# Optimization experiments

Hardware: AMD Instinct MI355X
Metric: run time of the kernel (lower is better)

The kernel has to match this reference:

```python
import math
import jax, jax.numpy as jnp
import numpy as np

B, S, H = 2, 2048, 1024
NH = 16
HD = H // NH            # 64
ROT = int(HD * 0.25)    # 16
QKV_SLOTS = 1024
PROJ_SLOTS = 1024
FFN_SLOTS = 4096
EPS = 1e-5


def gelu_l2_norm(x, axis=-1):
    # F.gelu (exact erf) then L2-normalize and rescale by sqrt(dim)
    g = jax.nn.gelu(x, approximate=False)
    n = jnp.linalg.norm(g, ord=2, axis=axis, keepdims=True)
    return g / n * math.sqrt(g.shape[axis])


def layer_norm(x, w, b):
    mu = jnp.mean(x, axis=-1, keepdims=True)
    var = jnp.mean(jnp.square(x - mu), axis=-1, keepdims=True)
    return (x - mu) * jax.lax.rsqrt(var + EPS) * w + b


def pattention(x, key_tok, val_tok):
    # [.., in] @ [slots, in]^T -> [.., slots]; NOTE: scale MULTIPLIES (as in source)
    aw = jnp.einsum('bsh,ph->bsp', x, key_tok) * math.sqrt(x.shape[-1])
    aw = gelu_l2_norm(aw, axis=-1)
    return jnp.einsum('bsp,pd->bsd', aw, val_tok)


def rotary_cos_sin(seq_len, rot_dim, base=10000.0):
    inv_freq = 1.0 / (base ** (jnp.arange(0, rot_dim, 2, dtype=jnp.float32) / rot_dim))
    t = jnp.arange(seq_len, dtype=jnp.float32)
    freqs = jnp.einsum('s,d->sd', t, inv_freq)           # [S, rot/2]
    emb = jnp.concatenate([freqs, freqs], axis=-1)       # [S, rot]
    return jnp.cos(emb), jnp.sin(emb)


def rotate_half(x):
    x1, x2 = jnp.split(x, 2, axis=-1)
    return jnp.concatenate([-x2, x1], axis=-1)


def setup_inputs() -> dict:
    key = jax.random.key(0)
    ks = jax.random.split(key, 12)
    p = lambda k, shape: jax.random.normal(k, shape, dtype=jnp.float32) * 0.02
    return {
        'x': jax.random.normal(ks[0], (B, S, H), dtype=jnp.float32),
        'ln1_w': jnp.ones((H,), jnp.float32), 'ln1_b': jnp.zeros((H,), jnp.float32),
        'ln2_w': jnp.ones((H,), jnp.float32), 'ln2_b': jnp.zeros((H,), jnp.float32),
        'q_key': p(ks[1], (QKV_SLOTS, H)), 'q_val': p(ks[2], (QKV_SLOTS, H)),
        'k_key': p(ks[3], (QKV_SLOTS, H)), 'k_val': p(ks[4], (QKV_SLOTS, H)),
        'v_key': p(ks[5], (QKV_SLOTS, H)), 'v_val': p(ks[6], (QKV_SLOTS, H)),
        'proj_key': p(ks[7], (PROJ_SLOTS, H)), 'proj_val': p(ks[8], (PROJ_SLOTS, H)),
        'ffn_key': p(ks[9], (FFN_SLOTS, H)), 'ffn_val': p(ks[10], (FFN_SLOTS, H)),
    }


def reference(x, ln1_w, ln1_b, ln2_w, ln2_b, q_key, q_val, k_key, k_val,
              v_key, v_val, proj_key, proj_val, ffn_key, ffn_val):
    residual = x
    xn = layer_norm(x, ln1_w, ln1_b)
    q = pattention(xn, q_key, q_val).reshape(B, S, NH, HD)
    k = pattention(xn, k_key, k_val).reshape(B, S, NH, HD)
    v = pattention(xn, v_key, v_val).reshape(B, S, NH, HD)

    cos, sin = rotary_cos_sin(S, ROT)          # [S, ROT]
    cos = cos[None, :, None, :]
    sin = sin[None, :, None, :]
    q_rot, q_pass = q[..., :ROT], q[..., ROT:]
    k_rot, k_pass = k[..., :ROT], k[..., ROT:]
    q_rot = q_rot * cos + rotate_half(q_rot) * sin
    k_rot = k_rot * cos + rotate_half(k_rot) * sin
    q = jnp.concatenate([q_rot, q_pass], axis=-1).transpose(0, 2, 1, 3)  # [B,NH,S,HD]
    k = jnp.concatenate([k_rot, k_pass], axis=-1).transpose(0, 2, 1, 3)
    v = v.transpose(0, 2, 1, 3)

    scale = math.sqrt(HD)
    causal = jnp.triu(jnp.ones((S, S), dtype=bool), k=1)
    attn_mask = jnp.where(causal, jnp.float32(-10000.0), jnp.float32(0.0))
    aw = jnp.einsum('bhqd,bhkd->bhqk', q, k) / scale + attn_mask
    aw = gelu_l2_norm(aw, axis=-1)
    o = jnp.einsum('bhqk,bhkd->bhqd', aw, v)
    o = o.transpose(0, 2, 1, 3).reshape(B, S, H)

    x = residual + pattention(o, proj_key, proj_val)
    residual = x
    x = residual + pattention(layer_norm(x, ln2_w, ln2_b), ffn_key, ffn_val)
    return x
```

## Files before the change

kernel.cpp:

```cpp
#include <hip/hip_runtime.h>

typedef __bf16 bf16x8 __attribute__((ext_vector_type(8)));
typedef float f32x4 __attribute__((ext_vector_type(4)));
typedef unsigned short u16;

__device__ __forceinline__ float b2f(u16 u) {
  union { unsigned int i; float f; } v; v.i = ((unsigned int)u) << 16; return v.f;
}
__device__ __forceinline__ u16 f2b(float f) {
  union { float f; unsigned int i; } v; v.f = f;
  unsigned int x = v.i;
  x += 0x7fffu + ((x >> 16) & 1u);
  return (u16)(x >> 16);
}
__device__ __forceinline__ float gelu_f(float x) {
  float x2 = x * x;
  float p = x * (1.5957691216f + 0.0713548162f * x2);
  float e = __expf(p);
  float r = __builtin_amdgcn_rcpf(1.0f + e);
  return x - x * r;
}
__device__ __forceinline__ void async16(const u16* g, u16* l) {
  __builtin_amdgcn_global_load_lds(
      (const __attribute__((address_space(1))) void*)g,
      (__attribute__((address_space(3))) void*)l, 16, 0, 0);
}
__device__ __forceinline__ void swz(int& bn, int& bm, int& bz) {
  int gx = (int)gridDim.x, gy = (int)gridDim.y;
  int flat = (int)(blockIdx.x + gridDim.x * (blockIdx.y + gridDim.y * blockIdx.z));
  int seq = flat >> 3;
  int nbm = gy >> 3;
  bm = (flat & 7) * nbm + seq % nbm;
  int rest = seq / nbm;
  bn = rest % gx;
  bz = rest / gx;
}

union U4 { uint4 u; u16 s[8]; };

__global__ __launch_bounds__(256) void cvt9_kernel(
    const float* __restrict__ qk, const float* __restrict__ kk,
    const float* __restrict__ vk, const float* __restrict__ pk,
    const float* __restrict__ fk, u16* __restrict__ w, float* __restrict__ ssqz) {
  int z = blockIdx.y;
  int i = blockIdx.x * 256 + threadIdx.x;
  if (z == 8) {
    if (i < 20480) ssqz[i] = 0.f;
    return;
  }
  const float* in = (z == 0) ? qk : (z == 1) ? kk : (z == 2) ? vk : (z == 3) ? pk
                    : fk + (size_t)(z - 4) * 1048576;
  u16* o = w + (size_t)z * 1048576;
  float4 f = ((const float4*)in)[i];
  ushort4 s;
  s.x = f2b(f.x); s.y = f2b(f.y); s.z = f2b(f.z); s.w = f2b(f.w);
  ((ushort4*)o)[i] = s;
}

__global__ __launch_bounds__(256) void cvtT8_kernel(
    const float* __restrict__ qv, const float* __restrict__ kv,
    const float* __restrict__ vv, const float* __restrict__ pv,
    const float* __restrict__ fv, u16* __restrict__ valsT, u16* __restrict__ fvT) {
  __shared__ float t[32][33];
  int z = blockIdx.z;
  const float* in; u16* o; int Rout, rowoff;
  if (z < 4) {
    in = (z == 0) ? qv : (z == 1) ? kv : (z == 2) ? vv : pv;
    o = valsT + (size_t)z * 1048576; Rout = 1024; rowoff = 0;
  } else {
    in = fv + (size_t)(z - 4) * 1048576;
    o = fvT; Rout = 4096; rowoff = (z - 4) * 1024;
  }
  int bc = blockIdx.x, br = blockIdx.y;
  int tid = threadIdx.x;
  int r = tid >> 5, cc = tid & 31;
  #pragma unroll
  for (int i = 0; i < 4; ++i)
    t[r + i * 8][cc] = in[(size_t)(br * 32 + r + i * 8) * 1024 + bc * 32 + cc];
  __syncthreads();
  #pragma unroll
  for (int i = 0; i < 4; ++i)
    o[(size_t)(bc * 32 + r + i * 8) * Rout + rowoff + br * 32 + cc] = f2b(t[cc][r + i * 8]);
}

__global__ __launch_bounds__(256) void ln_kernel(const float* __restrict__ x,
    const float* __restrict__ w, const float* __restrict__ b, u16* __restrict__ out) {
  int wv = threadIdx.x >> 6, lane = threadIdx.x & 63;
  int row = blockIdx.x * 4 + wv;
  const float* xr = x + (size_t)row * 1024;
  float4 v[4];
  float s = 0.f, s2 = 0.f;
  #pragma unroll
  for (int i = 0; i < 4; ++i) {
    v[i] = ((const float4*)xr)[lane + 64 * i];
    s += v[i].x + v[i].y + v[i].z + v[i].w;
    s2 += v[i].x * v[i].x + v[i].y * v[i].y + v[i].z * v[i].z + v[i].w * v[i].w;
  }
  #pragma unroll
  for (int m = 1; m < 64; m <<= 1) { s += __shfl_xor(s, m); s2 += __shfl_xor(s2, m); }
  float mu = s * (1.0f / 1024.0f);
  float inv = rsqrtf(s2 * (1.0f / 1024.0f) - mu * mu + 1e-5f);
  u16* orow = out + (size_t)row * 1024;
  #pragma unroll
  for (int i = 0; i < 4; ++i) {
    int c = (lane + 64 * i) * 4;
    ushort4 o;
    o.x = f2b((v[i].x - mu) * inv * w[c]     + b[c]);
    o.y = f2b((v[i].y - mu) * inv * w[c + 1] + b[c + 1]);
    o.z = f2b((v[i].z - mu) * inv * w[c + 2] + b[c + 2]);
    o.w = f2b((v[i].w - mu) * inv * w[c + 3] + b[c + 3]);
    ((ushort4*)orow)[lane + 64 * i] = o;
  }
}


template <int TM>
__global__ __launch_bounds__(256) void gemm_key(
    const u16* __restrict__ A, size_t sAz,
    const u16* __restrict__ B, size_t sBz,
    u16* __restrict__ C, size_t sCz,
    float* __restrict__ ssqb, size_t sSz,
    int N, int K, float alpha) {
  constexpr int AI = TM / 32;
  constexpr int G = TM / 64 + 2;
  __shared__ __align__(16) u16 As[3][TM * 32];
  __shared__ __align__(16) u16 Bs[3][128 * 32];
  int bn, bm, bz;
  swz(bn, bm, bz);
  const u16* Ab = A + (size_t)bz * sAz + (size_t)bm * TM * K;
  const u16* Bb = B + (size_t)bz * sBz + (size_t)bn * 128 * K;
  int tid = threadIdx.x, lane = tid & 63, wv = tid >> 6;
  int quad = lane >> 4, l16 = lane & 15;
  int lr = lane >> 2;
  int lcs = ((lane & 3) ^ ((lane >> 3) & 3)) * 8;
  int rq = quad ^ ((l16 >> 1) & 3);
  int wm = wv >> 1, wn = wv & 1;
  int RB = wm * (TM / 2), CB = wn * 64;
  auto STAGE = [&](int k0, int buf) {
    #pragma unroll
    for (int t = 0; t < TM / 64; ++t) {
      int ia = wv * (TM / 64) + t;
      async16(Ab + (size_t)(ia * 16 + lr) * K + k0 + lcs, &As[buf][ia * 512]);
    }
    #pragma unroll
    for (int t = 0; t < 2; ++t) {
      int ib = wv * 2 + t;
      async16(Bb + (size_t)(ib * 16 + lr) * K + k0 + lcs, &Bs[buf][ib * 512]);
    }
  };
  f32x4 zero = {0.f, 0.f, 0.f, 0.f};
  f32x4 acc[AI][4];
  #pragma unroll
  for (int i = 0; i < AI; ++i)
    #pragma unroll
    for (int j = 0; j < 4; ++j) acc[i][j] = zero;
  int NT = K >> 5;
  STAGE(0, 0);
  STAGE(32, 1);
  int cur = 0;
  for (int t = 0; t < NT; ++t) {
    if (t + 1 < NT) asm volatile("s_waitcnt vmcnt(%0)" :: "i"(G) : "memory");
    else            asm volatile("s_waitcnt vmcnt(0)" ::: "memory");
    __builtin_amdgcn_s_barrier();
    __builtin_amdgcn_sched_barrier(0);
    bf16x8 af[AI], bf[4];
    #pragma unroll
    for (int i = 0; i < AI; ++i)
      af[i] = *(const bf16x8*)&As[cur][(RB + i * 16 + l16) * 32 + rq * 8];
    #pragma unroll
    for (int j = 0; j < 4; ++j)
      bf[j] = *(const bf16x8*)&Bs[cur][(CB + j * 16 + l16) * 32 + rq * 8];
    if (t + 2 < NT) {
      int nb = cur + 2; if (nb >= 3) nb -= 3;
      STAGE((t + 2) * 32, nb);
    }
    #pragma unroll
    for (int i = 0; i < AI; ++i)
      #pragma unroll
      for (int j = 0; j < 4; ++j)
        acc[i][j] = __builtin_amdgcn_mfma_f32_16x16x32_bf16(af[i], bf[j], acc[i][j], 0, 0, 0);
    cur = (cur == 2) ? 0 : cur + 1;
  }
  #pragma unroll
  for (int i = 0; i < AI; ++i) {
    int rbase = bm * TM + RB + i * 16 + quad * 4;
    float srow[4] = {0.f, 0.f, 0.f, 0.f};
    #pragma unroll
    for (int j = 0; j < 4; ++j) {
      int c = bn * 128 + CB + j * 16 + l16;
      #pragma unroll
      for (int reg = 0; reg < 4; ++reg) {
        float g = gelu_f(acc[i][j][reg] * alpha);
        srow[reg] += g * g;
        C[(size_t)bz * sCz + (size_t)(rbase + reg) * N + c] = f2b(g);
      }
    }
    #pragma unroll
    for (int reg = 0; reg < 4; ++reg) {
      float s = srow[reg];
      s += __shfl_xor(s, 1); s += __shfl_xor(s, 2);
      s += __shfl_xor(s, 4); s += __shfl_xor(s, 8);
      if (l16 == 0) atomicAdd(&ssqb[bz * sSz + rbase + reg], s);
    }
  }
}

__global__ __launch_bounds__(256) void gemm_fkey(
    const u16* __restrict__ A,
    const u16* __restrict__ B,
    u16* __restrict__ C,
    float* __restrict__ ssqb,
    int N, int K, float alpha) {
  __shared__ __align__(16) u16 As[2][128 * 32];
  __shared__ __align__(16) u16 Bs[3][128 * 32];
  int bn, bm, bz;
  swz(bn, bm, bz);
  const u16* Ab = A + (size_t)bm * 128 * K;
  const u16* Bb = B + (size_t)bn * 128 * K;
  int tid = threadIdx.x, lane = tid & 63, wv = tid >> 6;
  int quad = lane >> 4, l16 = lane & 15;
  int lr = lane >> 2;
  int lcs = ((lane & 3) ^ ((lane >> 3) & 3)) * 8;
  int rq = quad ^ ((l16 >> 1) & 3);
  int wm = wv >> 1, wn = wv & 1;
  int RB = wm * 64, CB = wn * 64;
  auto STAGE_A = [&](int k0, int buf) {
    #pragma unroll
    for (int t = 0; t < 2; ++t) {
      int ia = wv * 2 + t;
      async16(Ab + (size_t)(ia * 16 + lr) * K + k0 + lcs, &As[buf][ia * 512]);
    }
  };
  auto STAGE_B = [&](int k0, int buf) {
    #pragma unroll
    for (int t = 0; t < 2; ++t) {
      int ib = wv * 2 + t;
      async16(Bb + (size_t)(ib * 16 + lr) * K + k0 + lcs, &Bs[buf][ib * 512]);
    }
  };
  f32x4 zero = {0.f, 0.f, 0.f, 0.f};
  f32x4 acc[4][4];
  #pragma unroll
  for (int i = 0; i < 4; ++i)
    #pragma unroll
    for (int j = 0; j < 4; ++j) acc[i][j] = zero;
  int NT = K >> 5;
  STAGE_A(0, 0);
  STAGE_B(0, 0);
  STAGE_B(32, 1);
  int cb = 0;
  for (int t = 0; t < NT; ++t) {
    if (t + 1 < NT) asm volatile("s_waitcnt vmcnt(2)" ::: "memory");
    else            asm volatile("s_waitcnt vmcnt(0)" ::: "memory");
    __builtin_amdgcn_s_barrier();
    __builtin_amdgcn_sched_barrier(0);
    bf16x8 af[4], bf[4];
    #pragma unroll
    for (int i = 0; i < 4; ++i)
      af[i] = *(const bf16x8*)&As[t & 1][(RB + i * 16 + l16) * 32 + rq * 8];
    #pragma unroll
    for (int j = 0; j < 4; ++j)
      bf[j] = *(const bf16x8*)&Bs[cb][(CB + j * 16 + l16) * 32 + rq * 8];
    if (t + 1 < NT) STAGE_A((t + 1) * 32, (t + 1) & 1);
    if (t + 2 < NT) {
      int nb = cb + 2; if (nb >= 3) nb -= 3;
      STAGE_B((t + 2) * 32, nb);
    }
    #pragma unroll
    for (int i = 0; i < 4; ++i)
      #pragma unroll
      for (int j = 0; j < 4; ++j)
        acc[i][j] = __builtin_amdgcn_mfma_f32_16x16x32_bf16(af[i], bf[j], acc[i][j], 0, 0, 0);
    cb = (cb == 2) ? 0 : cb + 1;
  }
  #pragma unroll
  for (int i = 0; i < 4; ++i) {
    int rbase = bm * 128 + RB + i * 16 + quad * 4;
    float srow[4] = {0.f, 0.f, 0.f, 0.f};
    #pragma unroll
    for (int j = 0; j < 4; ++j) {
      int c = bn * 128 + CB + j * 16 + l16;
      #pragma unroll
      for (int reg = 0; reg < 4; ++reg) {
        float g = gelu_f(acc[i][j][reg] * alpha);
        srow[reg] += g * g;
        C[(size_t)(rbase + reg) * N + c] = f2b(g);
      }
    }
    #pragma unroll
    for (int reg = 0; reg < 4; ++reg) {
      float s = srow[reg];
      s += __shfl_xor(s, 1); s += __shfl_xor(s, 2);
      s += __shfl_xor(s, 4); s += __shfl_xor(s, 8);
      if (l16 == 0) atomicAdd(&ssqb[rbase + reg], s);
    }
  }
}

template <int TM, int MODE, bool ROT>
__global__ __launch_bounds__(256) void gemm_val(
    const u16* __restrict__ A, size_t sAz,
    const u16* __restrict__ B, size_t sBz,
    void* __restrict__ C, size_t sCz,
    const float* __restrict__ ssqb, size_t sSz,
    int N, int K, int kzs, int klen, float sqrtP, const float* __restrict__ res) {
  constexpr int AI = TM / 32;
  constexpr int G = TM / 64 + 2;
  __shared__ __align__(16) u16 As[3][TM * 32];
  __shared__ __align__(16) u16 Bs[3][128 * 32];
  int bn, bm, bz;
  swz(bn, bm, bz);
  const u16* Ab = A + (size_t)bz * sAz + (size_t)bm * TM * K;
  const u16* Bb = B + (size_t)bz * sBz + (size_t)bn * 128 * K;
  int tid = threadIdx.x, lane = tid & 63, wv = tid >> 6;
  int quad = lane >> 4, l16 = lane & 15;
  int lr = lane >> 2;
  int lcs = ((lane & 3) ^ ((lane >> 3) & 3)) * 8;
  int rq = quad ^ ((l16 >> 1) & 3);
  int wm = wv >> 1, wn = wv & 1;
  int RB = wm * (TM / 2), CB = wn * 64;
  int kb0 = bz * kzs;
  auto STAGE = [&](int k0, int buf) {
    #pragma unroll
    for (int t = 0; t < TM / 64; ++t) {
      int ia = wv * (TM / 64) + t;
      async16(Ab + (size_t)(ia * 16 + lr) * K + kb0 + k0 + lcs, &As[buf][ia * 512]);
    }
    #pragma unroll
    for (int t = 0; t < 2; ++t) {
      int ib = wv * 2 + t;
      async16(Bb + (size_t)(ib * 16 + lr) * K + kb0 + k0 + lcs, &Bs[buf][ib * 512]);
    }
  };
  f32x4 zero = {0.f, 0.f, 0.f, 0.f};
  f32x4 acc[AI][4];
  #pragma unroll
  for (int i = 0; i < AI; ++i)
    #pragma unroll
    for (int j = 0; j < 4; ++j) acc[i][j] = zero;
  int NT = klen >> 5;
  STAGE(0, 0);
  STAGE(32, 1);
  int cur = 0;
  for (int t = 0; t < NT; ++t) {
    if (t + 1 < NT) asm volatile("s_waitcnt vmcnt(%0)" :: "i"(G) : "memory");
    else            asm volatile("s_waitcnt vmcnt(0)" ::: "memory");
    __builtin_amdgcn_s_barrier();
    __builtin_amdgcn_sched_barrier(0);
    bf16x8 af[AI], bf[4];
    #pragma unroll
    for (int i = 0; i < AI; ++i)
      af[i] = *(const bf16x8*)&As[cur][(RB + i * 16 + l16) * 32 + rq * 8];
    #pragma unroll
    for (int j = 0; j < 4; ++j)
      bf[j] = *(const bf16x8*)&Bs[cur][(CB + j * 16 + l16) * 32 + rq * 8];
    if (t + 2 < NT) {
      int nb = cur + 2; if (nb >= 3) nb -= 3;
      STAGE((t + 2) * 32, nb);
    }
    #pragma unroll
    for (int i = 0; i < AI; ++i)
      #pragma unroll
      for (int j = 0; j < 4; ++j)
        acc[i][j] = __builtin_amdgcn_mfma_f32_16x16x32_bf16(af[i], bf[j], acc[i][j], 0, 0, 0);
    cur = (cur == 2) ? 0 : cur + 1;
  }
  #pragma unroll
  for (int i = 0; i < AI; ++i) {
    int rbase = bm * TM + RB + i * 16 + quad * 4;
    float sc[4];
    if (MODE < 2) {
      #pragma unroll
      for (int reg = 0; reg < 4; ++reg)
        sc[reg] = sqrtP * rsqrtf(ssqb[bz * sSz + rbase + reg]);
    }
    #pragma unroll
    for (int j = 0; j < 4; ++j) {
      int c = bn * 128 + CB + j * 16 + l16;
      #pragma unroll
      for (int reg = 0; reg < 4; ++reg) {
        float v = acc[i][j][reg];
        size_t idx = (size_t)(rbase + reg) * N + c;
        if (MODE == 0) {
          float vs = v * sc[reg];
          if (ROT && j == 0) {
            float prt = __shfl_xor(vs, 8);
            if (bz < 2) {
              int seq = (rbase + reg) & 2047;
              float fr = exp2f((float)(l16 & 7) * -1.66096404744368f);
              float ang = (float)seq * fr;
              float c_ = __cosf(ang), s_ = __sinf(ang);
              vs = (l16 < 8) ? (vs * c_ - prt * s_) : (vs * c_ + prt * s_);
            }
          }
          ((u16*)C)[(size_t)bz * sCz + idx] = f2b(vs);
        } else if (MODE == 1) {
          ((float*)C)[idx] = v * sc[reg] + res[idx];
        } else {
          ((float*)C)[(size_t)bz * sCz + idx] = v;
        }
      }
    }
  }
}

__global__ __launch_bounds__(256) void vt_kernel(const u16* __restrict__ vb,
                                                 u16* __restrict__ vT) {
  __shared__ __align__(16) u16 T[64][72];
  int st = blockIdx.x, bh = blockIdx.y;
  int b = bh >> 4, h = bh & 15;
  int tid = threadIdx.x;
  #pragma unroll
  for (int i = 0; i < 2; ++i) {
    int l = tid + 256 * i;
    int s = l >> 3, dc = l & 7;
    *(uint4*)&T[s][dc * 8] =
        *(const uint4*)(vb + (size_t)(b * 2048 + st * 64 + s) * 1024 + h * 64 + dc * 8);
  }
  __syncthreads();
  #pragma unroll
  for (int i = 0; i < 2; ++i) {
    int l = tid + 256 * i;
    int d = l >> 3, scid = l & 7;
    int blk = (scid >> 2) * 32;
    int qq = (scid & 3) * 4;
    U4 u;
    #pragma unroll
    for (int j = 0; j < 8; ++j)
      u.s[j] = T[blk + (j >> 2) * 16 + qq + (j & 3)][d];
    *(uint4*)(vT + ((size_t)bh * 64 + d) * 2048 + st * 64 + scid * 8) = u.u;
  }
}

__global__ __launch_bounds__(256) void attn_kernel(
    const u16* __restrict__ qb, const u16* __restrict__ kb,
    const u16* __restrict__ vT, u16* __restrict__ ob) {
  __shared__ __align__(16) u16 Qs[64 * 64];
  __shared__ __align__(16) u16 Ks[2][64 * 64];
  __shared__ __align__(16) u16 Vts[2][64 * 64];
  int bh = blockIdx.x;
  int qt = 31 - (int)blockIdx.y;
  int b = bh >> 4, h = bh & 15;
  const u16* qp = qb + (size_t)b * 2048 * 1024 + h * 64;
  const u16* kp = kb + (size_t)b * 2048 * 1024 + h * 64;
  const u16* vp = vT + (size_t)bh * 64 * 2048;
  int tid = threadIdx.x, lane = tid & 63, wv = tid >> 6;
  int quad = lane >> 4, l16 = lane & 15;
  int lr8 = lane >> 3;
  int lc8s = ((lane & 7) ^ lr8) * 8;
  int rx = (l16 & 7) << 3;
  int MR = wv * 16;
  int nkt = qt + 1;
  #pragma unroll
  for (int t = 0; t < 2; ++t) {
    int idx = wv * 2 + t;
    async16(qp + (size_t)(qt * 64 + idx * 8 + lr8) * 1024 + lc8s, &Qs[idx * 512]);
    async16(kp + (size_t)(idx * 8 + lr8) * 1024 + lc8s, &Ks[0][idx * 512]);
    async16(vp + (size_t)(idx * 8 + lr8) * 2048 + lc8s, &Vts[0][idx * 512]);
  }
  f32x4 zero = {0.f, 0.f, 0.f, 0.f};
  f32x4 oacc[4];
  #pragma unroll
  for (int dn = 0; dn < 4; ++dn) oacc[dn] = zero;
  float ssql = 0.f;
  bf16x8 bq0 = {}, bq1 = {};
  for (int kt = 0, cur = 0; kt < nkt; ++kt, cur ^= 1) {
    __syncthreads();
    if (kt == 0) {
      bq0 = *(const bf16x8*)&Qs[((MR + l16) * 64 + quad * 8) ^ rx];
      bq1 = *(const bf16x8*)&Qs[((MR + l16) * 64 + 32 + quad * 8) ^ rx];
    }
    if (kt + 1 < nkt) {
      #pragma unroll
      for (int t = 0; t < 2; ++t) {
        int idx = wv * 2 + t;
        async16(kp + (size_t)((kt + 1) * 64 + idx * 8 + lr8) * 1024 + lc8s, &Ks[cur ^ 1][idx * 512]);
        async16(vp + (size_t)(idx * 8 + lr8) * 2048 + (kt + 1) * 64 + lc8s, &Vts[cur ^ 1][idx * 512]);
      }
    }
    bool dg = (kt == qt);
    #pragma unroll
    for (int kc = 0; kc < 2; ++kc) {
      bf16x8 pf;
      #pragma unroll
      for (int snh = 0; snh < 2; ++snh) {
        int sn = kc * 2 + snh;
        bf16x8 ak0 = *(const bf16x8*)&Ks[cur][((sn * 16 + l16) * 64 + quad * 8) ^ rx];
        bf16x8 ak1 = *(const bf16x8*)&Ks[cur][((sn * 16 + l16) * 64 + 32 + quad * 8) ^ rx];
        f32x4 st = zero;
        st = __builtin_amdgcn_mfma_f32_16x16x32_bf16(ak0, bq0, st, 0, 0, 0);
        st = __builtin_amdgcn_mfma_f32_16x16x32_bf16(ak1, bq1, st, 0, 0, 0);
        #pragma unroll
        for (int r = 0; r < 4; ++r) {
          float gl = gelu_f(st[r] * 0.125f);
          if (dg && (sn * 16 + quad * 4 + r > MR + l16)) gl = 0.f;
          ssql += gl * gl;
          pf[snh * 4 + r] = (__bf16)gl;
        }
      }
      #pragma unroll
      for (int dn = 0; dn < 4; ++dn) {
        bf16x8 bv = *(const bf16x8*)&Vts[cur][((dn * 16 + l16) * 64 + kc * 32 + quad * 8) ^ rx];
        oacc[dn] = __builtin_amdgcn_mfma_f32_16x16x32_bf16(pf, bv, oacc[dn], 0, 0, 0);
      }
    }
  }
  ssql += __shfl_xor(ssql, 16);
  ssql += __shfl_xor(ssql, 32);
  float sc = 45.254834f * rsqrtf(ssql);
  #pragma unroll
  for (int dn = 0; dn < 4; ++dn)
    #pragma unroll
    for (int r = 0; r < 4; ++r) {
      float scr = __shfl(sc, quad * 4 + r);
      int row = qt * 64 + MR + quad * 4 + r;
      int col = h * 64 + dn * 16 + l16;
      ob[(size_t)(b * 2048 + row) * 1024 + col] = f2b(oacc[dn][r] * scr);
    }
}

__global__ __launch_bounds__(256) void fin_kernel(
    const float* __restrict__ p0, const float* __restrict__ p1,
    const float* __restrict__ x1, const float* __restrict__ ssqf,
    float* __restrict__ out) {
  int row = blockIdx.x, t = threadIdx.x;
  float s = 64.0f * rsqrtf(ssqf[row]);
  size_t base = (size_t)row * 1024 + t * 4;
  float4 a = *(const float4*)(p0 + base);
  float4 b = *(const float4*)(p1 + base);
  float4 r = *(const float4*)(x1 + base);
  float4 o;
  o.x = r.x + s * (a.x + b.x); o.y = r.y + s * (a.y + b.y);
  o.z = r.z + s * (a.z + b.z); o.w = r.w + s * (a.w + b.w);
  *(float4*)(out + base) = o;
}

extern "C" void kernel_launch(void* const* d_in, const int* in_sizes, int n_in,
                              void* d_out, int out_size, void* d_ws, size_t ws_size,
                              hipStream_t stream) {
  const float* x    = (const float*)d_in[0];
  const float* ln1w = (const float*)d_in[1];
  const float* ln1b = (const float*)d_in[2];
  const float* ln2w = (const float*)d_in[3];
  const float* ln2b = (const float*)d_in[4];
  const float* qk   = (const float*)d_in[5];
  const float* qv   = (const float*)d_in[6];
  const float* kk   = (const float*)d_in[7];
  const float* kv   = (const float*)d_in[8];
  const float* vk   = (const float*)d_in[9];
  const float* vv   = (const float*)d_in[10];
  const float* pk   = (const float*)d_in[11];
  const float* pv   = (const float*)d_in[12];
  const float* fk   = (const float*)d_in[13];
  const float* fv   = (const float*)d_in[14];
  float* out = (float*)d_out;

  const size_t M1 = 1048576;
  u16* w = (u16*)d_ws;
  u16* wkeys  = w;
  u16* wpk    = w + 3 * M1;
  u16* wfk    = w + 4 * M1;
  u16* wvalsT = w + 8 * M1;
  u16* wpvT   = w + 11 * M1;
  u16* wfvT   = w + 12 * M1;
  u16* xn     = w + 16 * M1;
  u16* gq     = w + 20 * M1;
  u16* ob     = w + 20 * M1;
  u16* vT     = w + 24 * M1;
  u16* gp     = w + 28 * M1;
  u16* gf     = w + 20 * M1;
  u16* qb     = w + 36 * M1;
  u16* kb     = w + 40 * M1;
  u16* vb     = w + 44 * M1;
  float* ssq_qkv  = (float*)(w + 48 * M1);
  float* ssq_proj = ssq_qkv + 12288;
  float* ssq_ffn  = ssq_qkv + 16384;
  float* x1 = (float*)(w + 52 * M1);
  float* p0 = (float*)w;
  float* p1 = (float*)(w + 36 * M1);

  dim3 blk(256);
  cvt9_kernel<<<dim3(1024, 9), blk, 0, stream>>>(qk, kk, vk, pk, fk, w, ssq_qkv);
  cvtT8_kernel<<<dim3(32, 32, 8), blk, 0, stream>>>(qv, kv, vv, pv, fv, wvalsT, wfvT);

  ln_kernel<<<1024, blk, 0, stream>>>(x, ln1w, ln1b, xn);
  gemm_key<128><<<dim3(8, 32, 3), blk, 0, stream>>>(
      xn, 0, wkeys, M1, gq, 4 * M1, ssq_qkv, 4096, 1024, 1024, 32.0f);
  gemm_val<128, 0, true><<<dim3(8, 32, 3), blk, 0, stream>>>(
      gq, 4 * M1, wvalsT, M1, qb, 4 * M1, ssq_qkv, 4096, 1024, 1024, 0, 1024, 32.0f, nullptr);

  vt_kernel<<<dim3(32, 32), blk, 0, stream>>>(vb, vT);
  attn_kernel<<<dim3(32, 32), blk, 0, stream>>>(qb, kb, vT, ob);

  gemm_key<64><<<dim3(8, 64, 1), blk, 0, stream>>>(
      ob, 0, wpk, 0, gp, 0, ssq_proj, 0, 1024, 1024, 32.0f);
  gemm_val<64, 1, false><<<dim3(8, 64, 1), blk, 0, stream>>>(
      gp, 0, wpvT, 0, x1, 0, ssq_proj, 0, 1024, 1024, 0, 1024, 32.0f, x);

  ln_kernel<<<1024, blk, 0, stream>>>(x1, ln2w, ln2b, xn);
  gemm_fkey<<<dim3(32, 32, 1), blk, 0, stream>>>(
      xn, wfk, gf, ssq_ffn, 4096, 1024, 32.0f);
  gemm_val<128, 2, false><<<dim3(8, 32, 2), blk, 0, stream>>>(
      gf, 0, wfvT, 0, p0, 18 * M1, ssq_ffn, 0, 1024, 4096, 2048, 2048, 0.0f, nullptr);
  fin_kernel<<<4096, blk, 0, stream>>>(p0, p1, x1, ssq_ffn, out);
}
```

Baseline: 406.4 us.

## Fuse weight conversion and first layernorm into one prep kernel; widen FFN key GEMM tile

Merges the three startup kernels (weight bf16 conversion, value transposes, first layernorm) into a single launch that dispatches on a flat block index, removing two launch gaps. Separately, the FFN key GEMM tile grows from 128x128 to 128x256: each wave now computes 64x128 and B staging doubles. This halves the grid and improves reuse of A, at the cost of more accumulator registers (launch bounds set to 2 waves/SIMD) and more LDS.

Result: no change. 407.9 us (+0.4%).

```diff
diff --git a/kernel.cpp b/kernel.cpp
--- a/kernel.cpp
+++ b/kernel.cpp
@@ -38,49 +38,79 @@
 
 union U4 { uint4 u; u16 s[8]; };
 
-__global__ __launch_bounds__(256) void cvt9_kernel(
+__global__ __launch_bounds__(256) void prep_kernel(
     const float* __restrict__ qk, const float* __restrict__ kk,
     const float* __restrict__ vk, const float* __restrict__ pk,
-    const float* __restrict__ fk, u16* __restrict__ w, float* __restrict__ ssqz) {
-  int z = blockIdx.y;
-  int i = blockIdx.x * 256 + threadIdx.x;
-  if (z == 8) {
-    if (i < 20480) ssqz[i] = 0.f;
-    return;
-  }
-  const float* in = (z == 0) ? qk : (z == 1) ? kk : (z == 2) ? vk : (z == 3) ? pk
-                    : fk + (size_t)(z - 4) * 1048576;
-  u16* o = w + (size_t)z * 1048576;
-  float4 f = ((const float4*)in)[i];
-  ushort4 s;
-  s.x = f2b(f.x); s.y = f2b(f.y); s.z = f2b(f.z); s.w = f2b(f.w);
-  ((ushort4*)o)[i] = s;
-}
-
-__global__ __launch_bounds__(256) void cvtT8_kernel(
+    const float* __restrict__ fk, u16* __restrict__ w, float* __restrict__ ssqz,
     const float* __restrict__ qv, const float* __restrict__ kv,
     const float* __restrict__ vv, const float* __restrict__ pv,
-    const float* __restrict__ fv, u16* __restrict__ valsT, u16* __restrict__ fvT) {
+    const float* __restrict__ fv, u16* __restrict__ valsT, u16* __restrict__ fvT,
+    const float* __restrict__ x, const float* __restrict__ lnw,
+    const float* __restrict__ lnb, u16* __restrict__ xn) {
   __shared__ float t[32][33];
-  int z = blockIdx.z;
-  const float* in; u16* o; int Rout, rowoff;
-  if (z < 4) {
-    in = (z == 0) ? qv : (z == 1) ? kv : (z == 2) ? vv : pv;
-    o = valsT + (size_t)z * 1048576; Rout = 1024; rowoff = 0;
+  int id = (int)blockIdx.x;
+  int tid = threadIdx.x;
+  if (id < 9216) {
+    int z = id >> 10;
+    int i = (id & 1023) * 256 + tid;
+    if (z == 8) {
+      if (i < 20480) ssqz[i] = 0.f;
+      return;
+    }
+    const float* in = (z == 0) ? qk : (z == 1) ? kk : (z == 2) ? vk : (z == 3) ? pk
+                      : fk + (size_t)(z - 4) * 1048576;
+    u16* o = w + (size_t)z * 1048576;
+    float4 f = ((const float4*)in)[i];
+    ushort4 s;
+    s.x = f2b(f.x); s.y = f2b(f.y); s.z = f2b(f.z); s.w = f2b(f.w);
+    ((ushort4*)o)[i] = s;
+  } else if (id < 17408) {
+    int rid = id - 9216;
+    int bc = rid & 31, br = (rid >> 5) & 31, z = rid >> 10;
+    const float* in; u16* o; int Rout, rowoff;
+    if (z < 4) {
+      in = (z == 0) ? qv : (z == 1) ? kv : (z == 2) ? vv : pv;
+      o = valsT + (size_t)z * 1048576; Rout = 1024; rowoff = 0;
+    } else {
+      in = fv + (size_t)(z - 4) * 1048576;
+      o = fvT; Rout = 4096; rowoff = (z - 4) * 1024;
+    }
+    int r = tid >> 5, cc = tid & 31;
+    #pragma unroll
+    for (int i = 0; i < 4; ++i)
+      t[r + i * 8][cc] = in[(size_t)(br * 32 + r + i * 8) * 1024 + bc * 32 + cc];
+    __syncthreads();
+    #pragma unroll
+    for (int i = 0; i < 4; ++i)
+      o[(size_t)(bc * 32 + r + i * 8) * Rout + rowoff + br * 32 + cc] = f2b(t[cc][r + i * 8]);
   } else {
-    in = fv + (size_t)(z - 4) * 1048576;
-    o = fvT; Rout = 4096; rowoff = (z - 4) * 1024;
-  }
-  int bc = blockIdx.x, br = blockIdx.y;
-  int tid = threadIdx.x;
-  int r = tid >> 5, cc = tid & 31;
-  #pragma unroll
-  for (int i = 0; i < 4; ++i)
-    t[r + i * 8][cc] = in[(size_t)(br * 32 + r + i * 8) * 1024 + bc * 32 + cc];
-  __syncthreads();
-  #pragma unroll
-  for (int i = 0; i < 4; ++i)
-    o[(size_t)(bc * 32 + r + i * 8) * Rout + rowoff + br * 32 + cc] = f2b(t[cc][r + i * 8]);
+    int wv = tid >> 6, lane = tid & 63;
+    int row = (id - 17408) * 4 + wv;
+    const float* xr = x + (size_t)row * 1024;
+    float4 v[4];
+    float s = 0.f, s2 = 0.f;
+    #pragma unroll
+    for (int i = 0; i < 4; ++i) {
+      v[i] = ((const float4*)xr)[lane + 64 * i];
+      s += v[i].x + v[i].y + v[i].z + v[i].w;
+      s2 += v[i].x * v[i].x + v[i].y * v[i].y + v[i].z * v[i].z + v[i].w * v[i].w;
+    }
+    #pragma unroll
+    for (int m = 1; m < 64; m <<= 1) { s += __shfl_xor(s, m); s2 += __shfl_xor(s2, m); }
+    float mu = s * (1.0f / 1024.0f);
+    float inv = rsqrtf(s2 * (1.0f / 1024.0f) - mu * mu + 1e-5f);
+    u16* orow = xn + (size_t)row * 1024;
+    #pragma unroll
+    for (int i = 0; i < 4; ++i) {
+      int c = (lane + 64 * i) * 4;
+      ushort4 o;
+      o.x = f2b((v[i].x - mu) * inv * lnw[c]     + lnb[c]);
+      o.y = f2b((v[i].y - mu) * inv * lnw[c + 1] + lnb[c + 1]);
+      o.z = f2b((v[i].z - mu) * inv * lnw[c + 2] + lnb[c + 2]);
+      o.w = f2b((v[i].w - mu) * inv * lnw[c + 3] + lnb[c + 3]);
+      ((ushort4*)orow)[lane + 64 * i] = o;
+    }
+  }
 }
 
 __global__ __launch_bounds__(256) void ln_kernel(const float* __restrict__ x,
@@ -205,25 +235,25 @@
   }
 }
 
-__global__ __launch_bounds__(256) void gemm_fkey(
+__global__ __launch_bounds__(256, 2) void gemm_fkey(
     const u16* __restrict__ A,
     const u16* __restrict__ B,
     u16* __restrict__ C,
     float* __restrict__ ssqb,
     int N, int K, float alpha) {
   __shared__ __align__(16) u16 As[2][128 * 32];
-  __shared__ __align__(16) u16 Bs[3][128 * 32];
+  __shared__ __align__(16) u16 Bs[3][256 * 32];
   int bn, bm, bz;
   swz(bn, bm, bz);
   const u16* Ab = A + (size_t)bm * 128 * K;
-  const u16* Bb = B + (size_t)bn * 128 * K;
+  const u16* Bb = B + (size_t)bn * 256 * K;
   int tid = threadIdx.x, lane = tid & 63, wv = tid >> 6;
   int quad = lane >> 4, l16 = lane & 15;
   int lr = lane >> 2;
   int lcs = ((lane & 3) ^ ((lane >> 3) & 3)) * 8;
   int rq = quad ^ ((l16 >> 1) & 3);
   int wm = wv >> 1, wn = wv & 1;
-  int RB = wm * 64, CB = wn * 64;
+  int RB = wm * 64, CB = wn * 128;
   auto STAGE_A = [&](int k0, int buf) {
     #pragma unroll
     for (int t = 0; t < 2; ++t) {
@@ -233,33 +263,33 @@
   };
   auto STAGE_B = [&](int k0, int buf) {
     #pragma unroll
-    for (int t = 0; t < 2; ++t) {
-      int ib = wv * 2 + t;
+    for (int t = 0; t < 4; ++t) {
+      int ib = wv * 4 + t;
       async16(Bb + (size_t)(ib * 16 + lr) * K + k0 + lcs, &Bs[buf][ib * 512]);
     }
   };
   f32x4 zero = {0.f, 0.f, 0.f, 0.f};
-  f32x4 acc[4][4];
+  f32x4 acc[4][8];
   #pragma unroll
   for (int i = 0; i < 4; ++i)
     #pragma unroll
-    for (int j = 0; j < 4; ++j) acc[i][j] = zero;
+    for (int j = 0; j < 8; ++j) acc[i][j] = zero;
   int NT = K >> 5;
   STAGE_A(0, 0);
   STAGE_B(0, 0);
   STAGE_B(32, 1);
   int cb = 0;
   for (int t = 0; t < NT; ++t) {
-    if (t + 1 < NT) asm volatile("s_waitcnt vmcnt(2)" ::: "memory");
+    if (t + 1 < NT) asm volatile("s_waitcnt vmcnt(4)" ::: "memory");
     else            asm volatile("s_waitcnt vmcnt(0)" ::: "memory");
     __builtin_amdgcn_s_barrier();
     __builtin_amdgcn_sched_barrier(0);
-    bf16x8 af[4], bf[4];
+    bf16x8 af[4], bf[8];
     #pragma unroll
     for (int i = 0; i < 4; ++i)
       af[i] = *(const bf16x8*)&As[t & 1][(RB + i * 16 + l16) * 32 + rq * 8];
     #pragma unroll
-    for (int j = 0; j < 4; ++j)
+    for (int j = 0; j < 8; ++j)
       bf[j] = *(const bf16x8*)&Bs[cb][(CB + j * 16 + l16) * 32 + rq * 8];
     if (t + 1 < NT) STAGE_A((t + 1) * 32, (t + 1) & 1);
     if (t + 2 < NT) {
@@ -269,7 +299,7 @@
     #pragma unroll
     for (int i = 0; i < 4; ++i)
       #pragma unroll
-      for (int j = 0; j < 4; ++j)
+      for (int j = 0; j < 8; ++j)
         acc[i][j] = __builtin_amdgcn_mfma_f32_16x16x32_bf16(af[i], bf[j], acc[i][j], 0, 0, 0);
     cb = (cb == 2) ? 0 : cb + 1;
   }
@@ -278,8 +308,8 @@
     int rbase = bm * 128 + RB + i * 16 + quad * 4;
     float srow[4] = {0.f, 0.f, 0.f, 0.f};
     #pragma unroll
-    for (int j = 0; j < 4; ++j) {
-      int c = bn * 128 + CB + j * 16 + l16;
+    for (int j = 0; j < 8; ++j) {
+      int c = bn * 256 + CB + j * 16 + l16;
       #pragma unroll
       for (int reg = 0; reg < 4; ++reg) {
         float g = gelu_f(acc[i][j][reg] * alpha);
@@ -580,10 +610,11 @@
   float* p1 = (float*)(w + 36 * M1);
 
   dim3 blk(256);
-  cvt9_kernel<<<dim3(1024, 9), blk, 0, stream>>>(qk, kk, vk, pk, fk, w, ssq_qkv);
-  cvtT8_kernel<<<dim3(32, 32, 8), blk, 0, stream>>>(qv, kv, vv, pv, fv, wvalsT, wfvT);
-
-  ln_kernel<<<1024, blk, 0, stream>>>(x, ln1w, ln1b, xn);
+  prep_kernel<<<18432, blk, 0, stream>>>(
+      qk, kk, vk, pk, fk, w, ssq_qkv,
+      qv, kv, vv, pv, fv, wvalsT, wfvT,
+      x, ln1w, ln1b, xn);
+
   gemm_key<128><<<dim3(8, 32, 3), blk, 0, stream>>>(
       xn, 0, wkeys, M1, gq, 4 * M1, ssq_qkv, 4096, 1024, 1024, 32.0f);
   gemm_val<128, 0, true><<<dim3(8, 32, 3), blk, 0, stream>>>(
@@ -598,7 +629,7 @@
       gp, 0, wpvT, 0, x1, 0, ssq_proj, 0, 1024, 1024, 0, 1024, 32.0f, x);
 
   ln_kernel<<<1024, blk, 0, stream>>>(x1, ln2w, ln2b, xn);
-  gemm_fkey<<<dim3(32, 32, 1), blk, 0, stream>>>(
+  gemm_fkey<<<dim3(16, 32, 1), blk, 0, stream>>>(
       xn, wfk, gf, ssq_ffn, 4096, 1024, 32.0f);
   gemm_val<128, 2, false><<<dim3(8, 32, 2), blk, 0, stream>>>(
       gf, 0, wfvT, 0, p0, 18 * M1, ssq_ffn, 0, 1024, 4096, 2048, 2048, 0.0f, nullptr);
```
